# Performance work log

Hardware: AMD Instinct MI355X
Metric: run time of the kernel (lower is better)

The kernel has to match this reference:

```python
import jax, jax.numpy as jnp
import numpy as np

EPS = 1e-5

def _conv(x, w, stride=1, pad=0, groups=1):
    return jax.lax.conv_general_dilated(x, w, (stride, stride), [(pad, pad), (pad, pad)],
                                        dimension_numbers=('NCHW', 'OIHW', 'NCHW'),
                                        feature_group_count=groups)

def _bn(x, g, b, m, v):
    # eval-mode BatchNorm2d with running stats
    return g[None, :, None, None] * (x - m[None, :, None, None]) / jnp.sqrt(v[None, :, None, None] + EPS) + b[None, :, None, None]

def setup_inputs():
    key = jax.random.key(0)
    ks = jax.random.split(key, 16)
    B, C, H = 32, 1024, 28
    G, Cg, Sq = 16, 64, 256  # groups, channels-per-group, SE squeeze width
    f32 = jnp.float32
    def bn_params(k):
        k1, k2, k3, k4 = jax.random.split(k, 4)
        return (jax.random.uniform(k1, (C,), f32, 0.5, 1.5),
                jax.random.normal(k2, (C,), f32) * 0.1,
                jax.random.normal(k3, (C,), f32) * 0.1,
                jax.random.uniform(k4, (C,), f32, 0.5, 1.5))
    ga, ba, ma, va = bn_params(ks[0])
    gb, bb, mb, vb = bn_params(ks[1])
    gc, bc, mc, vc = bn_params(ks[2])
    return dict(
        x=jax.random.normal(ks[3], (B, C, H, H), f32),
        temperature=1,
        wa=jax.random.normal(ks[4], (C, C, 1, 1), f32) * 0.03,
        ga=ga, ba=ba, ma=ma, va=va,
        wb=jax.random.normal(ks[5], (C, Cg, 3, 3), f32) * 0.04,
        gb=gb, bb=bb, mb=mb, vb=vb,
        sw1=jax.random.normal(ks[6], (Sq, C, 1, 1), f32) * 0.03, sb1=jnp.zeros((Sq,), f32),
        sw2=jax.random.normal(ks[7], (C, Sq, 1, 1), f32) * 0.06, sb2=jnp.zeros((C,), f32),
        wc=jax.random.normal(ks[8], (C, C, 1, 1), f32) * 0.03,
        gc=gc, bc=bc, mc=mc, vc=vc,
        mkw=jax.random.normal(ks[9], (2, C, 1, 1), f32) * 0.1,
        mkb=jnp.array([10.0, 0.0], f32) + jax.random.normal(ks[10], (2,), f32),
    )

def reference(x, temperature, wa, ga, ba, ma, va, wb, gb, bb, mb, vb,
              sw1, sb1, sw2, sb2, wc, gc, bc, mc, vc, mkw, mkb):
    B, C, H, W = x.shape
    ms = 7; r = H // ms; G = 16  # mask_size, upsample ratio, conv groups
    # ---- Masker (eval mode): adaptive avg-pool 28->7, 1x1 conv to 2 logit maps, hard select
    pooled = x.reshape(B, C, ms, r, ms, r).mean(axis=(3, 5))          # [B,C,7,7]
    logits = _conv(pooled, mkw) + mkb[None, :, None, None]            # [B,2,7,7]
    logits = logits.reshape(B, 2, 1, ms, ms)
    mask = (logits[:, 0] >= logits[:, 1]).astype(x.dtype)             # [B,1,7,7]
    sparsity = mask.mean()
    mask = jnp.repeat(jnp.repeat(mask, r, axis=2), r, axis=3)         # nearest upsample -> [B,1,28,28]
    # ExpandMask (stride=1): 3x3 all-ones conv, pad 1, threshold
    mask_dil = _conv(mask, jnp.ones((1, 1, 3, 3), x.dtype), pad=1) > 0.5
    sparsity_dil = mask_dil.astype(x.dtype).mean()
    mask_flops = C * ms * ms + (2 * C + C) * ms * ms  # as in source flops bookkeeping
    # ---- Bottleneck transform: 1x1 -> 3x3 grouped -> SE -> 1x1
    h = jax.nn.relu(_bn(_conv(x, wa), ga, ba, ma, va))
    h = jax.nn.relu(_bn(_conv(h, wb, pad=1, groups=G), gb, bb, mb, vb))
    s = h.mean(axis=(2, 3), keepdims=True)                            # SE squeeze
    s = jax.nn.relu(_conv(s, sw1) + sb1[None, :, None, None])
    s = jax.nn.sigmoid(_conv(s, sw2) + sb2[None, :, None, None])
    h = h * s
    h = _bn(_conv(h, wc), gc, bc, mc, vc)
    h = h * mask                                                      # apply_mask (g==1: broadcast)
    out = jax.nn.relu(h + x)                                          # identity residual (no proj)
    # ---- flops / sparsity bookkeeping (returned like the torch module)
    c1 = C * C; c2 = C * C * 9 // G; c3 = C * C
    dense = mask_flops + (c1 + c2 + c3) * H * W
    sparse = mask_flops + c1 * H * W * sparsity_dil + (c2 + c3) * H * W * sparsity
    perc = sparse / dense
    return (out, sparsity[None], sparsity_dil[None], perc[None], sparse)
```

## Files before the change

kernel.cpp:

```cpp
#include <hip/hip_runtime.h>

typedef __bf16 bf16;
typedef __bf16 bf16x8 __attribute__((ext_vector_type(8)));
typedef __bf16 bf16x4 __attribute__((ext_vector_type(4)));
typedef float  f32x4  __attribute__((ext_vector_type(4)));

#define EPSBN 1e-5f

__device__ __forceinline__ void gload16(const void* gp, void* lp) {
  __builtin_amdgcn_global_load_lds(
      (__attribute__((address_space(1))) void*)(unsigned long long)gp,
      (__attribute__((address_space(3))) void*)(unsigned)(unsigned long long)lp,
      16, 0, 0);
}

__global__ __launch_bounds__(256) void k_init(
    const float* __restrict__ wa, const float* __restrict__ wc, const float* __restrict__ wb,
    const float* __restrict__ ga, const float* __restrict__ ba, const float* __restrict__ ma, const float* __restrict__ va,
    const float* __restrict__ gb, const float* __restrict__ bb, const float* __restrict__ mb, const float* __restrict__ vb,
    const float* __restrict__ gc, const float* __restrict__ bc, const float* __restrict__ mc, const float* __restrict__ vc,
    bf16* __restrict__ wa_bf, bf16* __restrict__ wc_bf, bf16* __restrict__ wb_bf,
    float* __restrict__ bn6, float* __restrict__ sums, unsigned* __restrict__ cnts,
    bf16* __restrict__ h1p)
{
  const int bid = blockIdx.x, tid = threadIdx.x;
  if (bid < 1024) {
    unsigned i = bid * 256 + tid;
    unsigned e = i * 4;
    float4 a = *(const float4*)(wa + e);
    bf16x4 av; av[0]=(bf16)a.x; av[1]=(bf16)a.y; av[2]=(bf16)a.z; av[3]=(bf16)a.w;
    *(bf16x4*)(wa_bf + e) = av;
    float4 c = *(const float4*)(wc + e);
    bf16x4 cv; cv[0]=(bf16)c.x; cv[1]=(bf16)c.y; cv[2]=(bf16)c.z; cv[3]=(bf16)c.w;
    *(bf16x4*)(wc_bf + e) = cv;
    if (i < 1024) {
      float s;
      s = ga[i] / sqrtf(va[i] + EPSBN); bn6[i]        = s; bn6[1024 + i] = ba[i] - ma[i] * s;
      s = gb[i] / sqrtf(vb[i] + EPSBN); bn6[2048 + i] = s; bn6[3072 + i] = bb[i] - mb[i] * s;
      s = gc[i] / sqrtf(vc[i] + EPSBN); bn6[4096 + i] = s; bn6[5120 + i] = bc[i] - mc[i] * s;
    }
    if (i < 32768) sums[i] = 0.f;
    if (i == 0) { cnts[0] = 0u; cnts[1] = 0u; }
  } else if (bid < 3328) {
    int t = (bid - 1024) * 256 + tid;
    int ci = t & 63;
    int u  = t >> 6;
    int cl = u & 63;
    int gk = u >> 6;
    int g  = gk / 9, kk = gk - g * 9;
    wb_bf[t] = (bf16)wb[(((size_t)(g * 64 + cl) * 64) + ci) * 9 + kk];
  } else {
    int t = (bid - 3328) * 256 + tid;
    int c8 = t & 127;
    int r  = (t >> 7) % 116;
    int b  = t / (116 * 128);
    int y, x;
    if (r < 30)      { y = 0;      x = r; }
    else if (r < 60) { y = 29;     x = r - 30; }
    else if (r < 88) { y = r - 59; x = 0; }
    else             { y = r - 87; x = 29; }
    size_t off = (((size_t)b * 30 + y) * 30 + x) * 1024 + (size_t)c8 * 8;
    *(uint4*)(h1p + off) = uint4{0, 0, 0, 0};
  }
}

__global__ __launch_bounds__(256) void k_cast_pool(
    const float* __restrict__ x, bf16* __restrict__ xT, bf16* __restrict__ pooledb)
{
  const int pt = blockIdx.x, ct = blockIdx.y, b = blockIdx.z;
  __shared__ float tile[64 * 116];
  const int tid = threadIdx.x;
  const float* src = x + ((size_t)(b * 1024 + ct * 64)) * 784 + pt * 112;
  #pragma unroll
  for (int it = 0; it < 7; it++) {
    unsigned f = tid + it * 256;
    unsigned ci = f / 28, j = f % 28;
    float4 v = *(const float4*)(src + (size_t)ci * 784 + j * 4);
    *(float4*)(tile + ci * 116 + j * 4) = v;
  }
  __syncthreads();
  bf16* dst = xT + ((size_t)(b * 784 + pt * 112)) * 1024 + ct * 64;
  for (int s = tid; s < 896; s += 256) {
    int j = s >> 3, c8 = s & 7;
    bf16x8 tmp;
    #pragma unroll
    for (int e = 0; e < 8; e++) tmp[e] = (bf16)tile[(c8 * 8 + e) * 116 + j];
    *(bf16x8*)(dst + (size_t)j * 1024 + c8 * 8) = tmp;
  }
  for (int s = tid; s < 448; s += 256) {
    int c = s / 7, ox = s % 7;
    float acc = 0.f;
    #pragma unroll
    for (int yy = 0; yy < 4; yy++)
      #pragma unroll
      for (int xx = 0; xx < 4; xx++)
        acc += tile[c * 116 + yy * 28 + ox * 4 + xx];
    pooledb[((size_t)b * 49 + pt * 7 + ox) * 1024 + ct * 64 + c] = (bf16)(acc * (1.0f / 16.0f));
  }
}

__global__ __launch_bounds__(256) void k_mask(
    const bf16* __restrict__ pooledb, const float* __restrict__ mkw, const float* __restrict__ mkb,
    float* __restrict__ mask7, unsigned* __restrict__ cnts)
{
  const int b = blockIdx.x, tid = threadIdx.x;
  const int lane = tid & 63, w = tid >> 6;
  __shared__ float l0s[49], l1s[49];
  __shared__ unsigned char m7[56];
  float w0r[16], w1r[16];
  #pragma unroll
  for (int i = 0; i < 4; i++) {
    *(f32x4*)(w0r + i * 4) = *(const f32x4*)(mkw + lane * 16 + i * 4);
    *(f32x4*)(w1r + i * 4) = *(const f32x4*)(mkw + 1024 + lane * 16 + i * 4);
  }
  const float mkb0 = mkb[0], mkb1 = mkb[1];
  for (int p = w; p < 49; p += 4) {
    const bf16* pp = pooledb + ((size_t)b * 49 + p) * 1024 + lane * 16;
    bf16x8 h0 = *(const bf16x8*)pp;
    bf16x8 h1 = *(const bf16x8*)(pp + 8);
    float a0 = 0.f, a1 = 0.f;
    #pragma unroll
    for (int e = 0; e < 8; e++) {
      float v0 = (float)h0[e], v1 = (float)h1[e];
      a0 += v0 * w0r[e] + v1 * w0r[8 + e];
      a1 += v0 * w1r[e] + v1 * w1r[8 + e];
    }
    #pragma unroll
    for (int d = 1; d < 64; d <<= 1) { a0 += __shfl_xor(a0, d); a1 += __shfl_xor(a1, d); }
    if (lane == 0) { l0s[p] = a0 + mkb0; l1s[p] = a1 + mkb1; }
  }
  __syncthreads();
  if (tid < 49) {
    unsigned char m = (l0s[tid] >= l1s[tid]) ? 1 : 0;
    m7[tid] = m;
    mask7[b * 49 + tid] = (float)m;
  }
  __syncthreads();
  if (tid < 64) {
    unsigned long long bal = __ballot((tid < 49) && m7[tid]);
    if (tid == 0) atomicAdd(&cnts[0], (unsigned)__popcll(bal));
  }
  int cnt = 0;
  for (int p2 = tid; p2 < 784; p2 += 256) {
    int y = p2 / 28, x = p2 % 28;
    int cy0 = (y == 0) ? 0 : (y - 1) >> 2, cy1 = (y == 27) ? 6 : (y + 1) >> 2;
    int cx0 = (x == 0) ? 0 : (x - 1) >> 2, cx1 = (x == 27) ? 6 : (x + 1) >> 2;
    int d = 0;
    for (int cy = cy0; cy <= cy1; cy++)
      for (int cx = cx0; cx <= cx1; cx++) d |= m7[cy * 7 + cx];
    cnt += d;
  }
  #pragma unroll
  for (int d = 1; d < 64; d <<= 1) cnt += __shfl_xor(cnt, d);
  __shared__ int wsum[4];
  if (lane == 0) wsum[w] = cnt;
  __syncthreads();
  if (tid == 0) atomicAdd(&cnts[1], (unsigned)(wsum[0] + wsum[1] + wsum[2] + wsum[3]));
}

__global__ void k_fin(const unsigned* __restrict__ cnts, float* __restrict__ tail)
{
  if (threadIdx.x == 0 && blockIdx.x == 0) {
    float sp = (float)cnts[0] / 1568.0f;
    float sd = (float)cnts[1] / 25088.0f;
    const float c1 = 1048576.0f, c2 = 589824.0f, c3 = 1048576.0f, mf = 200704.0f;
    float dense  = mf + (c1 + c2 + c3) * 784.0f;
    float sparse = mf + c1 * 784.0f * sd + (c2 + c3) * 784.0f * sp;
    tail[0] = sp; tail[1] = sd; tail[2] = sparse / dense; tail[3] = sparse;
  }
}

template<int MODE>
__global__ __launch_bounds__(256) void k_gemm(
    const bf16* __restrict__ Aop, const bf16* __restrict__ Bop, void* __restrict__ outp,
    const float* __restrict__ bn6, const float* __restrict__ xres,
    const float* __restrict__ mask7)
{
  int id = blockIdx.x, pixt, cot;
  if (id < 1536) { pixt = (id >> 6) * 8 + (id & 7); cot = (id >> 3) & 7; }
  else { int wi = id - 1536; pixt = 192 + (wi & 3); cot = wi >> 2; }
  const int mt = (MODE == 0) ? cot : pixt;
  const int nt = (MODE == 0) ? pixt : cot;

  __shared__ bf16 ldsA[8192];
  __shared__ bf16 ldsB[8192];
  const int tid = threadIdx.x, lane = tid & 63, w = tid >> 6;
  const int wm = w & 1, wn = w >> 1;
  const int li = lane & 15, q = lane >> 4;

  const bf16* Ab = Aop + (size_t)mt * 128 * 1024;
  const bf16* Bb = Bop + (size_t)nt * 128 * 1024;
  const bf16* ga[4]; const bf16* gb[4];
  #pragma unroll
  for (int j = 0; j < 4; j++) {
    int c = w * 256 + j * 64 + lane;
    int row = c >> 3, k8 = (c & 7) ^ (row & 7);
    ga[j] = Ab + (size_t)row * 1024 + k8 * 8;
    gb[j] = Bb + (size_t)row * 1024 + k8 * 8;
  }
  const int lb = li * 128 + ((q ^ (li & 7)) << 4);
  f32x4 acc[4][4] = {};

  for (int kt = 0; kt < 16; kt++) {
    #pragma unroll
    for (int j = 0; j < 4; j++) gload16(ga[j], (char*)ldsA + w * 4096 + j * 1024);
    #pragma unroll
    for (int j = 0; j < 4; j++) gload16(gb[j], (char*)ldsB + w * 4096 + j * 1024);
    #pragma unroll
    for (int j = 0; j < 4; j++) { ga[j] += 64; gb[j] += 64; }
    __syncthreads();
    #pragma unroll
    for (int ks = 0; ks < 2; ks++) {
      bf16x8 af[4], bfr[4];
      #pragma unroll
      for (int m = 0; m < 4; m++)
        af[m] = *(const bf16x8*)((const char*)ldsA + wm * 8192 + m * 2048 + (lb ^ (ks * 64)));
      #pragma unroll
      for (int n = 0; n < 4; n++)
        bfr[n] = *(const bf16x8*)((const char*)ldsB + wn * 8192 + n * 2048 + (lb ^ (ks * 64)));
      #pragma unroll
      for (int m = 0; m < 4; m++)
        #pragma unroll
        for (int n = 0; n < 4; n++)
          acc[m][n] = __builtin_amdgcn_mfma_f32_16x16x32_bf16(af[m], bfr[n], acc[m][n], 0, 0, 0);
    }
    __syncthreads();
  }

  if constexpr (MODE == 0) {
    bf16* h1p = (bf16*)outp;
    const int co0 = mt * 128 + wm * 64 + q * 4;
    f32x4 sv[4], ov[4];
    #pragma unroll
    for (int m = 0; m < 4; m++) {
      sv[m] = *(const f32x4*)(bn6 + co0 + m * 16);
      ov[m] = *(const f32x4*)(bn6 + 1024 + co0 + m * 16);
    }
    #pragma unroll
    for (int n = 0; n < 4; n++) {
      unsigned p = nt * 128 + wn * 64 + n * 16 + li;
      unsigned b = p / 784u, rem = p % 784u;
      unsigned y = rem / 28u, xx = rem % 28u;
      bf16* dst = h1p + (((size_t)b * 30 + y + 1) * 30 + xx + 1) * 1024 + co0;
      #pragma unroll
      for (int m = 0; m < 4; m++) {
        bf16x4 pk;
        #pragma unroll
        for (int r = 0; r < 4; r++)
          pk[r] = (bf16)fmaxf(acc[m][n][r] * sv[m][r] + ov[m][r], 0.f);
        *(bf16x4*)(dst + m * 16) = pk;
      }
    }
  } else {
    float* dst = (float*)outp;
    const int p0 = mt * 128 + wm * 64 + q * 4;
    int bM[4]; unsigned hwM[4]; float mvv[4];
    #pragma unroll
    for (int m = 0; m < 4; m++) {
      int pm = p0 + m * 16;
      int b = pm / 784; unsigned hw = pm - b * 784;
      bM[m] = b; hwM[m] = hw;
      unsigned y = hw / 28u, xx = hw % 28u;
      mvv[m] = mask7[b * 49 + (y >> 2) * 7 + (xx >> 2)];
    }
    #pragma unroll
    for (int n = 0; n < 4; n++) {
      int co = nt * 128 + wn * 64 + n * 16 + li;
      float s = bn6[4096 + co], o = bn6[5120 + co];
      #pragma unroll
      for (int m = 0; m < 4; m++) {
        size_t base = ((size_t)(bM[m] * 1024 + co)) * 784 + hwM[m];
        f32x4 xv = *(const f32x4*)(xres + base);
        f32x4 rv;
        #pragma unroll
        for (int r = 0; r < 4; r++) {
          float v = acc[m][n][r] * s + o;
          rv[r] = fmaxf(v * mvv[m] + xv[r], 0.f);
        }
        *(f32x4*)(dst + base) = rv;
      }
    }
  }
}

__global__ __launch_bounds__(256) void k_conv_b(
    const bf16* __restrict__ h1p, const bf16* __restrict__ wb_bf,
    bf16* __restrict__ h2T, float* __restrict__ sums, const float* __restrict__ bn6)
{
  const int b = blockIdx.x, g = blockIdx.y, yt = blockIdx.z;
  __shared__ bf16 ldsI[184 * 64];
  const int tid = threadIdx.x, lane = tid & 63, w = tid >> 6;
  const int li = lane & 15, q = lane >> 4;

  bf16x8 wreg[9][2];
  #pragma unroll
  for (int kk = 0; kk < 9; kk++)
    #pragma unroll
    for (int cs = 0; cs < 2; cs++)
      wreg[kk][cs] = *(const bf16x8*)(wb_bf +
          (((size_t)(g * 9 + kk) * 64) + w * 16 + li) * 64 + cs * 32 + q * 8);

  const bf16* iBase = h1p + (size_t)b * 921600 + (size_t)(4 * yt) * 30 * 1024 + g * 64;
  #pragma unroll
  for (int t = 0; t < 6; t++) {
    int j = w + t * 4;
    if (j < 23 && (j < 22 || lane < 32)) {
      int c = j * 64 + lane;
      int pos = c >> 3, ci8 = (c & 7) ^ (pos & 7);
      gload16(iBase + (size_t)pos * 1024 + ci8 * 8, (char*)ldsI + j * 1024);
    }
  }

  int pos0[7];
  #pragma unroll
  for (int mtt = 0; mtt < 7; mtt++) {
    int n = mtt * 16 + li;
    pos0[mtt] = (n / 28) * 30 + (n % 28);
  }
  __syncthreads();

  f32x4 acc[7] = {};
  #pragma unroll
  for (int kk = 0; kk < 9; kk++) {
    const int shift = (kk / 3) * 30 + (kk % 3);
    #pragma unroll
    for (int cs = 0; cs < 2; cs++) {
      #pragma unroll
      for (int mtt = 0; mtt < 7; mtt++) {
        int pos = pos0[mtt] + shift;
        int off = pos * 128 + ((((cs << 2) + q) ^ (pos & 7)) << 4);
        bf16x8 ifr = *(const bf16x8*)((const char*)ldsI + off);
        acc[mtt] = __builtin_amdgcn_mfma_f32_16x16x32_bf16(wreg[kk][cs], ifr, acc[mtt], 0, 0, 0);
      }
    }
  }

  const int co4 = g * 64 + w * 16 + q * 4;
  f32x4 sv = *(const f32x4*)(bn6 + 2048 + co4);
  f32x4 ov = *(const f32x4*)(bn6 + 3072 + co4);
  f32x4 csum = {0.f, 0.f, 0.f, 0.f};
  #pragma unroll
  for (int mtt = 0; mtt < 7; mtt++) {
    int pl = yt * 112 + mtt * 16 + li;
    bf16x4 pk;
    #pragma unroll
    for (int r = 0; r < 4; r++) {
      float v = fmaxf(acc[mtt][r] * sv[r] + ov[r], 0.f);
      csum[r] += v;
      pk[r] = (bf16)v;
    }
    *(bf16x4*)(h2T + ((size_t)b * 784 + pl) * 1024 + co4) = pk;
  }
  #pragma unroll
  for (int d = 1; d < 16; d <<= 1) {
    #pragma unroll
    for (int r = 0; r < 4; r++) csum[r] += __shfl_xor(csum[r], d);
  }
  if (li == 0) {
    #pragma unroll
    for (int r = 0; r < 4; r++) atomicAdd(&sums[b * 1024 + co4 + r], csum[r]);
  }
}

__global__ __launch_bounds__(256) void k_se1(
    const float* __restrict__ sums, const float* __restrict__ sw1, const float* __restrict__ sb1,
    float* __restrict__ s1g)
{
  const int sqc = blockIdx.x, b = blockIdx.y, tid = threadIdx.x;
  __shared__ float mean[1024];
  for (int i = tid; i < 1024; i += 256) mean[i] = sums[b * 1024 + i] * (1.0f / 784.0f);
  __syncthreads();
  const int row = sqc * 32 + (tid >> 3), part = tid & 7;
  const f32x4* wr = (const f32x4*)(sw1 + (size_t)row * 1024 + part * 128);
  const float* mr = mean + part * 128;
  float acc = 0.f;
  #pragma unroll 8
  for (int i = 0; i < 32; i++) {
    f32x4 wv = wr[i];
    acc += wv[0] * mr[i * 4] + wv[1] * mr[i * 4 + 1] + wv[2] * mr[i * 4 + 2] + wv[3] * mr[i * 4 + 3];
  }
  acc += __shfl_xor(acc, 1); acc += __shfl_xor(acc, 2); acc += __shfl_xor(acc, 4);
  if (part == 0) s1g[b * 256 + row] = fmaxf(acc + sb1[row], 0.f);
}

__global__ __launch_bounds__(256) void k_se2(
    const float* __restrict__ s1g, const float* __restrict__ sw2, const float* __restrict__ sb2,
    float* __restrict__ s2)
{
  const int coc = blockIdx.x, b = blockIdx.y, tid = threadIdx.x;
  __shared__ float s1s[256];
  s1s[tid] = s1g[b * 256 + tid];
  __syncthreads();
  const int co = coc * 256 + tid;
  const f32x4* wr = (const f32x4*)(sw2 + (size_t)co * 256);
  float acc = sb2[co];
  #pragma unroll 8
  for (int i = 0; i < 64; i++) {
    f32x4 wv = wr[i];
    acc += wv[0] * s1s[i * 4] + wv[1] * s1s[i * 4 + 1] + wv[2] * s1s[i * 4 + 2] + wv[3] * s1s[i * 4 + 3];
  }
  s2[b * 1024 + co] = 1.0f / (1.0f + __expf(-acc));
}

__global__ __launch_bounds__(256) void k_scale(bf16* __restrict__ h2T, const float* __restrict__ s2)
{
  size_t idx = ((size_t)blockIdx.x * 256 + threadIdx.x) * 8;
  unsigned b = (unsigned)(idx / 802816u);
  unsigned c = (unsigned)(idx & 1023u);
  const float* sp = s2 + b * 1024 + c;
  bf16x8 v = *(const bf16x8*)(h2T + idx);
  #pragma unroll
  for (int e = 0; e < 8; e++) v[e] = (bf16)((float)v[e] * sp[e]);
  *(bf16x8*)(h2T + idx) = v;
}

extern "C" void kernel_launch(void* const* d_in, const int* in_sizes, int n_in,
                              void* d_out, int out_size, void* d_ws, size_t ws_size,
                              hipStream_t stream)
{
  const float* x   = (const float*)d_in[0];
  const float* wa  = (const float*)d_in[2];
  const float* ga  = (const float*)d_in[3];
  const float* ba  = (const float*)d_in[4];
  const float* ma  = (const float*)d_in[5];
  const float* va  = (const float*)d_in[6];
  const float* wb  = (const float*)d_in[7];
  const float* gb  = (const float*)d_in[8];
  const float* bb  = (const float*)d_in[9];
  const float* mb  = (const float*)d_in[10];
  const float* vb  = (const float*)d_in[11];
  const float* sw1 = (const float*)d_in[12];
  const float* sb1 = (const float*)d_in[13];
  const float* sw2 = (const float*)d_in[14];
  const float* sb2 = (const float*)d_in[15];
  const float* wc  = (const float*)d_in[16];
  const float* gc  = (const float*)d_in[17];
  const float* bc  = (const float*)d_in[18];
  const float* mc  = (const float*)d_in[19];
  const float* vc  = (const float*)d_in[20];
  const float* mkw = (const float*)d_in[21];
  const float* mkb = (const float*)d_in[22];

  char* ws = (char*)d_ws;
  bf16*  xT      = (bf16*)(ws + 0);
  bf16*  h1p     = (bf16*)(ws + 51380224);
  bf16*  wa_bf   = (bf16*)(ws + 110362624);
  bf16*  wc_bf   = (bf16*)(ws + 112459776);
  bf16*  wb_bf   = (bf16*)(ws + 114556928);
  bf16*  pooledb = (bf16*)(ws + 115736576);
  float* mask7   = (float*)(ws + 118947840);
  float* sums    = (float*)(ws + 118956032);
  float* s1g     = (float*)(ws + 119087104);
  float* s2      = (float*)(ws + 119119872);
  float* bn6     = (float*)(ws + 119250944);
  unsigned* cnts = (unsigned*)(ws + 119275520);

  float* out = (float*)d_out;

  k_init<<<5184, 256, 0, stream>>>(wa, wc, wb, ga, ba, ma, va, gb, bb, mb, vb, gc, bc, mc, vc,
                                   wa_bf, wc_bf, wb_bf, bn6, sums, cnts, h1p);
  k_cast_pool<<<dim3(7, 16, 32), 256, 0, stream>>>(x, xT, pooledb);
  k_mask<<<32, 256, 0, stream>>>(pooledb, mkw, mkb, mask7, cnts);
  k_fin<<<1, 64, 0, stream>>>(cnts, out + 25690112);
  k_gemm<0><<<1568, 256, 0, stream>>>(wa_bf, xT, h1p, bn6, nullptr, nullptr);
  k_conv_b<<<dim3(32, 16, 7), 256, 0, stream>>>(h1p, wb_bf, xT , sums, bn6);
  k_se1<<<dim3(8, 32), 256, 0, stream>>>(sums, sw1, sb1, s1g);
  k_se2<<<dim3(4, 32), 256, 0, stream>>>(s1g, sw2, sb2, s2);
  k_scale<<<12544, 256, 0, stream>>>(xT, s2);
  k_gemm<1><<<1568, 256, 0, stream>>>(xT , wc_bf, out, bn6, x, mask7);
}
```

Measured before the change: 502.0 us.

## Retile grouped 3x3 conv to 8 rows per block and fold k_fin into SE

The grouped 3x3 conv block now covers 8 output rows instead of 4, with each wave handling half the rows and 32 output channels. Each LDS input fragment therefore feeds two MFMAs, and halo loading is amortized over more pixels. The tail-row tile masks out unused fragments. The tiny k_fin launch is merged into k_se2, and the GEMM template is wrapped in named kernels. The trade-offs are more accumulator registers, fewer blocks (4 y-tiles instead of 7), and load imbalance on the last tile.

New measurement: 511.9 us. Within noise of the previous version (+2.0%).

```diff
diff --git a/kernel.cpp b/kernel.cpp
--- a/kernel.cpp
+++ b/kernel.cpp
@@ -158,20 +158,8 @@
   if (tid == 0) atomicAdd(&cnts[1], (unsigned)(wsum[0] + wsum[1] + wsum[2] + wsum[3]));
 }
 
-__global__ void k_fin(const unsigned* __restrict__ cnts, float* __restrict__ tail)
-{
-  if (threadIdx.x == 0 && blockIdx.x == 0) {
-    float sp = (float)cnts[0] / 1568.0f;
-    float sd = (float)cnts[1] / 25088.0f;
-    const float c1 = 1048576.0f, c2 = 589824.0f, c3 = 1048576.0f, mf = 200704.0f;
-    float dense  = mf + (c1 + c2 + c3) * 784.0f;
-    float sparse = mf + c1 * 784.0f * sd + (c2 + c3) * 784.0f * sp;
-    tail[0] = sp; tail[1] = sd; tail[2] = sparse / dense; tail[3] = sparse;
-  }
-}
-
 template<int MODE>
-__global__ __launch_bounds__(256) void k_gemm(
+__device__ __forceinline__ void gemm_body(
     const bf16* __restrict__ Aop, const bf16* __restrict__ Bop, void* __restrict__ outp,
     const float* __restrict__ bn6, const float* __restrict__ xres,
     const float* __restrict__ mask7)
@@ -283,28 +271,36 @@
   }
 }
 
+__global__ __launch_bounds__(256) void k_conv_a(
+    const bf16* __restrict__ A, const bf16* __restrict__ B, void* __restrict__ o,
+    const float* __restrict__ bn6)
+{ gemm_body<0>(A, B, o, bn6, nullptr, nullptr); }
+
+__global__ __launch_bounds__(256) void k_conv_c(
+    const bf16* __restrict__ A, const bf16* __restrict__ B, void* __restrict__ o,
+    const float* __restrict__ bn6, const float* __restrict__ xres, const float* __restrict__ mask7)
+{ gemm_body<1>(A, B, o, bn6, xres, mask7); }
+
 __global__ __launch_bounds__(256) void k_conv_b(
     const bf16* __restrict__ h1p, const bf16* __restrict__ wb_bf,
     bf16* __restrict__ h2T, float* __restrict__ sums, const float* __restrict__ bn6)
 {
   const int b = blockIdx.x, g = blockIdx.y, yt = blockIdx.z;
-  __shared__ bf16 ldsI[184 * 64];
+  __shared__ bf16 ldsI[300 * 64];
   const int tid = threadIdx.x, lane = tid & 63, w = tid >> 6;
   const int li = lane & 15, q = lane >> 4;
-
-  bf16x8 wreg[9][2];
-  #pragma unroll
-  for (int kk = 0; kk < 9; kk++)
-    #pragma unroll
-    for (int cs = 0; cs < 2; cs++)
-      wreg[kk][cs] = *(const bf16x8*)(wb_bf +
-          (((size_t)(g * 9 + kk) * 64) + w * 16 + li) * 64 + cs * 32 + q * 8);
-
-  const bf16* iBase = h1p + (size_t)b * 921600 + (size_t)(4 * yt) * 30 * 1024 + g * 64;
-  #pragma unroll
-  for (int t = 0; t < 6; t++) {
+  const int h = w >> 1, cg2 = w & 1;
+
+  const bool full = (yt < 3);
+  const int fullC  = full ? 37 : 22;
+  const int mcount = full ? 7 : (h ? 3 : 4);
+  const int mbase  = full ? h * 7 : (h ? 4 : 0);
+
+  const bf16* iBase = h1p + (size_t)b * 921600 + (size_t)(8 * yt) * 30 * 1024 + g * 64;
+  #pragma unroll
+  for (int t = 0; t < 10; t++) {
     int j = w + t * 4;
-    if (j < 23 && (j < 22 || lane < 32)) {
+    if (j < fullC || (j == fullC && lane < 32)) {
       int c = j * 64 + lane;
       int pos = c >> 3, ci8 = (c & 7) ^ (pos & 7);
       gload16(iBase + (size_t)pos * 1024 + ci8 * 8, (char*)ldsI + j * 1024);
@@ -313,52 +309,76 @@
 
   int pos0[7];
   #pragma unroll
-  for (int mtt = 0; mtt < 7; mtt++) {
-    int n = mtt * 16 + li;
-    pos0[mtt] = (n / 28) * 30 + (n % 28);
-  }
-  __syncthreads();
-
-  f32x4 acc[7] = {};
-  #pragma unroll
-  for (int kk = 0; kk < 9; kk++) {
-    const int shift = (kk / 3) * 30 + (kk % 3);
-    #pragma unroll
-    for (int cs = 0; cs < 2; cs++) {
-      #pragma unroll
-      for (int mtt = 0; mtt < 7; mtt++) {
-        int pos = pos0[mtt] + shift;
-        int off = pos * 128 + ((((cs << 2) + q) ^ (pos & 7)) << 4);
-        bf16x8 ifr = *(const bf16x8*)((const char*)ldsI + off);
-        acc[mtt] = __builtin_amdgcn_mfma_f32_16x16x32_bf16(wreg[kk][cs], ifr, acc[mtt], 0, 0, 0);
+  for (int i = 0; i < 7; i++) {
+    int p = (mbase + i) * 16 + li;
+    pos0[i] = (p / 28) * 30 + (p % 28);
+  }
+  __syncthreads();
+
+  f32x4 acc[7][2] = {};
+  const bf16* wbase = wb_bf + ((size_t)g * 9 * 64 + cg2 * 32 + li) * 64 + q * 8;
+  #pragma unroll
+  for (int cs = 0; cs < 2; cs++) {
+    bf16x8 wcs[9][2];
+    #pragma unroll
+    for (int kk = 0; kk < 9; kk++)
+      #pragma unroll
+      for (int c2 = 0; c2 < 2; c2++)
+        wcs[kk][c2] = *(const bf16x8*)(wbase + ((size_t)kk * 64 + c2 * 16) * 64 + cs * 32);
+    #pragma unroll
+    for (int kk = 0; kk < 9; kk++) {
+      const int shift = (kk / 3) * 30 + (kk % 3);
+      #pragma unroll
+      for (int i = 0; i < 7; i++) {
+        if (i < mcount) {
+          int pos = pos0[i] + shift;
+          int off = pos * 128 + ((((cs << 2) + q) ^ (pos & 7)) << 4);
+          bf16x8 ifr = *(const bf16x8*)((const char*)ldsI + off);
+          acc[i][0] = __builtin_amdgcn_mfma_f32_16x16x32_bf16(wcs[kk][0], ifr, acc[i][0], 0, 0, 0);
+          acc[i][1] = __builtin_amdgcn_mfma_f32_16x16x32_bf16(wcs[kk][1], ifr, acc[i][1], 0, 0, 0);
+        }
       }
     }
   }
 
-  const int co4 = g * 64 + w * 16 + q * 4;
-  f32x4 sv = *(const f32x4*)(bn6 + 2048 + co4);
-  f32x4 ov = *(const f32x4*)(bn6 + 3072 + co4);
-  f32x4 csum = {0.f, 0.f, 0.f, 0.f};
-  #pragma unroll
-  for (int mtt = 0; mtt < 7; mtt++) {
-    int pl = yt * 112 + mtt * 16 + li;
-    bf16x4 pk;
-    #pragma unroll
-    for (int r = 0; r < 4; r++) {
-      float v = fmaxf(acc[mtt][r] * sv[r] + ov[r], 0.f);
-      csum[r] += v;
-      pk[r] = (bf16)v;
-    }
-    *(bf16x4*)(h2T + ((size_t)b * 784 + pl) * 1024 + co4) = pk;
-  }
-  #pragma unroll
-  for (int d = 1; d < 16; d <<= 1) {
-    #pragma unroll
-    for (int r = 0; r < 4; r++) csum[r] += __shfl_xor(csum[r], d);
-  }
+  const int cobase = g * 64 + cg2 * 32;
+  f32x4 sv[2], ov[2], csum[2];
+  #pragma unroll
+  for (int c2 = 0; c2 < 2; c2++) {
+    sv[c2] = *(const f32x4*)(bn6 + 2048 + cobase + c2 * 16 + q * 4);
+    ov[c2] = *(const f32x4*)(bn6 + 3072 + cobase + c2 * 16 + q * 4);
+    csum[c2] = f32x4{0.f, 0.f, 0.f, 0.f};
+  }
+  #pragma unroll
+  for (int i = 0; i < 7; i++) {
+    if (i < mcount) {
+      int pl = yt * 224 + (mbase + i) * 16 + li;
+      bf16* dst = h2T + ((size_t)b * 784 + pl) * 1024 + cobase + q * 4;
+      #pragma unroll
+      for (int c2 = 0; c2 < 2; c2++) {
+        bf16x4 pk;
+        #pragma unroll
+        for (int r = 0; r < 4; r++) {
+          float v = fmaxf(acc[i][c2][r] * sv[c2][r] + ov[c2][r], 0.f);
+          csum[c2][r] += v;
+          pk[r] = (bf16)v;
+        }
+        *(bf16x4*)(dst + c2 * 16) = pk;
+      }
+    }
+  }
+  #pragma unroll
+  for (int d = 1; d < 16; d <<= 1)
+    #pragma unroll
+    for (int c2 = 0; c2 < 2; c2++)
+      #pragma unroll
+      for (int r = 0; r < 4; r++) csum[c2][r] += __shfl_xor(csum[c2][r], d);
   if (li == 0) {
     #pragma unroll
-    for (int r = 0; r < 4; r++) atomicAdd(&sums[b * 1024 + co4 + r], csum[r]);
+    for (int c2 = 0; c2 < 2; c2++)
+      #pragma unroll
+      for (int r = 0; r < 4; r++)
+        atomicAdd(&sums[b * 1024 + cobase + c2 * 16 + q * 4 + r], csum[c2][r]);
   }
 }
 
@@ -385,9 +405,17 @@
 
 __global__ __launch_bounds__(256) void k_se2(
     const float* __restrict__ s1g, const float* __restrict__ sw2, const float* __restrict__ sb2,
-    float* __restrict__ s2)
+    float* __restrict__ s2, const unsigned* __restrict__ cnts, float* __restrict__ tail)
 {
   const int coc = blockIdx.x, b = blockIdx.y, tid = threadIdx.x;
+  if (coc == 0 && b == 0 && tid == 0) {
+    float sp = (float)cnts[0] / 1568.0f;
+    float sd = (float)cnts[1] / 25088.0f;
+    const float c1 = 1048576.0f, c2 = 589824.0f, c3 = 1048576.0f, mf = 200704.0f;
+    float dense  = mf + (c1 + c2 + c3) * 784.0f;
+    float sparse = mf + c1 * 784.0f * sd + (c2 + c3) * 784.0f * sp;
+    tail[0] = sp; tail[1] = sd; tail[2] = sparse / dense; tail[3] = sparse;
+  }
   __shared__ float s1s[256];
   s1s[tid] = s1g[b * 256 + tid];
   __syncthreads();
@@ -461,11 +489,10 @@
                                    wa_bf, wc_bf, wb_bf, bn6, sums, cnts, h1p);
   k_cast_pool<<<dim3(7, 16, 32), 256, 0, stream>>>(x, xT, pooledb);
   k_mask<<<32, 256, 0, stream>>>(pooledb, mkw, mkb, mask7, cnts);
-  k_fin<<<1, 64, 0, stream>>>(cnts, out + 25690112);
-  k_gemm<0><<<1568, 256, 0, stream>>>(wa_bf, xT, h1p, bn6, nullptr, nullptr);
-  k_conv_b<<<dim3(32, 16, 7), 256, 0, stream>>>(h1p, wb_bf, xT , sums, bn6);
+  k_conv_a<<<1568, 256, 0, stream>>>(wa_bf, xT, h1p, bn6);
+  k_conv_b<<<dim3(32, 16, 4), 256, 0, stream>>>(h1p, wb_bf, xT , sums, bn6);
   k_se1<<<dim3(8, 32), 256, 0, stream>>>(sums, sw1, sb1, s1g);
-  k_se2<<<dim3(4, 32), 256, 0, stream>>>(s1g, sw2, sb2, s2);
+  k_se2<<<dim3(4, 32), 256, 0, stream>>>(s1g, sw2, sb2, s2, cnts, out + 25690112);
   k_scale<<<12544, 256, 0, stream>>>(xT, s2);
-  k_gemm<1><<<1568, 256, 0, stream>>>(xT , wc_bf, out, bn6, x, mask7);
-}
+  k_conv_c<<<1568, 256, 0, stream>>>(xT , wc_bf, out, bn6, x, mask7);
+}
```
